# Kernel optimization log

Hardware: AMD Instinct MI355X
Metric: run time of the kernel (lower is better)

Reference implementation:

```python
import jax, jax.numpy as jnp
import numpy as np

B, T, F = 64, 512, 256
ENC = 256      # encoder output dim
P = 128        # projection_dim
H = 256        # gru_hidden_dim
K = 12         # num_future_steps
TEMP = 0.1


def setup_inputs() -> dict:
    key = jax.random.key(0)
    ks = jax.random.split(key, 12)
    s = lambda *d: 1.0 / np.sqrt(d[0])
    return {
        "x_seq": jax.random.normal(ks[0], (B, T, F), jnp.float32),
        # encoder: Dense(F -> ENC)
        "W_enc": jax.random.normal(ks[1], (F, ENC), jnp.float32) * s(F),
        "b_enc": jnp.zeros((ENC,), jnp.float32),
        # projection: Dense(ENC -> P)
        "W_proj": jax.random.normal(ks[2], (ENC, P), jnp.float32) * s(ENC),
        "b_proj": jnp.zeros((P,), jnp.float32),
        # GRUCell (flax convention: input dense has bias, hidden dense bias only on n)
        "Wi": jax.random.normal(ks[3], (P, 3 * H), jnp.float32) * s(P),
        "bi": jnp.zeros((3 * H,), jnp.float32),
        "Wh": jax.random.normal(ks[4], (H, 3 * H), jnp.float32) * s(H),
        "bhn": jnp.zeros((H,), jnp.float32),
        # K predictors: Dense(H -> P)
        "Wp": jax.random.normal(ks[5], (K, H, P), jnp.float32) * s(H),
        "bp": jnp.zeros((K, P), jnp.float32),
    }


def _gru_scan(z_seq, Wi, bi, Wh, bhn):
    # z_seq: [B, T, P] -> c_seq: [B, T, H]
    def step(h, x_t):
        gi = x_t @ Wi + bi          # [B, 3H]
        gh = h @ Wh                 # [B, 3H]
        ir, iz, inn = jnp.split(gi, 3, axis=-1)
        hr, hz, hn = jnp.split(gh, 3, axis=-1)
        r = jax.nn.sigmoid(ir + hr)
        z = jax.nn.sigmoid(iz + hz)
        n = jnp.tanh(inn + r * (hn + bhn))
        h_new = (1.0 - z) * n + z * h
        return h_new, h_new

    h0 = jnp.zeros((z_seq.shape[0], Wh.shape[0]), z_seq.dtype)
    _, c = jax.lax.scan(step, h0, jnp.swapaxes(z_seq, 0, 1))  # c: [T, B, H]
    return jnp.swapaxes(c, 0, 1)


def reference(x_seq, W_enc, b_enc, W_proj, b_proj, Wi, bi, Wh, bhn, Wp, bp):
    # encoder per timestep (vmap(vmap(Dense)) == batched matmul)
    z_seq = x_seq @ W_enc + b_enc                 # [B, T, ENC]
    z_seq = z_seq @ W_proj + b_proj               # [B, T, P]
    c_seq = _gru_scan(z_seq, Wi, bi, Wh, bhn)     # [B, T, H]

    Tlen = z_seq.shape[1]
    loss = jnp.asarray(0.0, z_seq.dtype)
    for k in range(1, K + 1):
        if Tlen - k <= 0:
            continue
        z_pos = z_seq[:, k:]                      # [B, T-k, P]
        pred = c_seq[:, :-k] @ Wp[k - 1] + bp[k - 1]  # [B, T-k, P]
        logits = jnp.einsum('btd,bkd->btk', pred, z_pos) / TEMP
        labels = jnp.arange(logits.shape[1])
        # NOTE: faithful to source: [..., labels] with labels=arange is an
        # identity gather along the last axis (not a diagonal pick).
        loss = loss + jnp.mean(-jax.nn.log_softmax(logits, axis=-1)[..., labels])
    return loss / K
```

## Files before the change

kernel.cpp:

```cpp
#include <hip/hip_runtime.h>
#include <hip/hip_bf16.h>
#include <math.h>

#define B_   64
#define T_   512
#define F_   256
#define ENC_ 256
#define P_   128
#define H_   256
#define K_   12
#define INV_TEMP 10.0f

typedef unsigned short u16;
typedef _Float16 half2v __attribute__((ext_vector_type(2)));
union U2H { unsigned int u; half2v h; };
typedef __attribute__((ext_vector_type(8))) short bf16x8;
typedef __attribute__((ext_vector_type(4))) float f32x4;
typedef _Float16 f16x8 __attribute__((ext_vector_type(8)));
union BF8 { bf16x8 v; u16 e[8]; };

__device__ __forceinline__ float rcpf(float x) {
#if __has_builtin(__builtin_amdgcn_rcpf)
    return __builtin_amdgcn_rcpf(x);
#else
    return 1.f / x;
#endif
}
__device__ __forceinline__ u16 f2bf(float f) {
    unsigned int u = __float_as_uint(f);
    unsigned int r = (u + 0x7fffu + ((u >> 16) & 1u)) >> 16;
    return (u16)r;
}
__device__ __forceinline__ float bf2f(u16 v) {
    return __uint_as_float(((unsigned int)v) << 16);
}
__device__ __forceinline__ float bflo(unsigned int u) { return __uint_as_float(u << 16); }
__device__ __forceinline__ float bfhi(unsigned int u) { return __uint_as_float(u & 0xffff0000u); }
__device__ __forceinline__ float wave_sum(float v) {
    #pragma unroll
    for (int o = 32; o > 0; o >>= 1) v += __shfl_down(v, o, 64);
    return v;
}

__global__ __launch_bounds__(256) void setup_conv(const float* __restrict__ Wh,
                                                  _Float16* __restrict__ Wht,
                                                  const float* __restrict__ Wi,
                                                  u16* __restrict__ Wit,
                                                  const float* __restrict__ Wp,
                                                  u16* __restrict__ Wpt,
                                                  const float* __restrict__ We,
                                                  const float* __restrict__ be,
                                                  const float* __restrict__ Wpj,
                                                  const float* __restrict__ bpj,
                                                  u16* __restrict__ Wct,
                                                  float* __restrict__ bc,
                                                  float* __restrict__ accum) {
    int bid = blockIdx.x;
    if (bid < 192) {
        __shared__ float tile0[32][33];
        int g0 = (bid % 24) * 32, k0 = (bid / 24) * 32;
        int tx = threadIdx.x & 31, ty = threadIdx.x >> 5;
        #pragma unroll
        for (int i = 0; i < 32; i += 8)
            tile0[ty + i][tx] = Wh[(size_t)(k0 + ty + i) * 768 + g0 + tx];
        __syncthreads();
        #pragma unroll
        for (int i = 0; i < 32; i += 8)
            Wht[(size_t)(g0 + ty + i) * 256 + k0 + tx] = (_Float16)tile0[tx][ty + i];
    } else if (bid < 288) {
        __shared__ float tile[32][33];
        int b2 = bid - 192;
        int n0 = (b2 % 24) * 32, k0 = (b2 / 24) * 32;
        int tx = threadIdx.x & 31, ty = threadIdx.x >> 5;
        #pragma unroll
        for (int i = 0; i < 32; i += 8)
            tile[ty + i][tx] = Wi[(size_t)(k0 + ty + i) * 768 + n0 + tx];
        __syncthreads();
        #pragma unroll
        for (int i = 0; i < 32; i += 8)
            Wit[(size_t)(n0 + ty + i) * 128 + k0 + tx] = f2bf(tile[tx][ty + i]);
    } else if (bid < 672) {
        __shared__ float tile2[32][33];
        int b3 = bid - 288;
        int kq = b3 / 32, rem = b3 % 32;
        int h0 = (rem % 8) * 32, p0 = (rem / 8) * 32;
        int tx = threadIdx.x & 31, ty = threadIdx.x >> 5;
        #pragma unroll
        for (int i = 0; i < 32; i += 8)
            tile2[ty + i][tx] = Wp[(size_t)kq * H_ * P_ + (size_t)(h0 + ty + i) * P_ + p0 + tx];
        __syncthreads();
        #pragma unroll
        for (int i = 0; i < 32; i += 8)
            Wpt[(size_t)kq * P_ * H_ + (size_t)(p0 + ty + i) * H_ + h0 + tx] = f2bf(tile2[tx][ty + i]);
    } else {
        int f = (bid - 672) * 2 + (threadIdx.x >> 7);
        int p = threadIdx.x & 127;
        if (f < F_) {
            float a = 0.f;
            for (int e = 0; e < ENC_; e++) a = fmaf(We[f * ENC_ + e], Wpj[e * P_ + p], a);
            Wct[(size_t)p * F_ + f] = f2bf(a);
        } else if (f == F_) {
            float a = bpj[p];
            for (int e = 0; e < ENC_; e++) a = fmaf(be[e], Wpj[e * P_ + p], a);
            bc[p] = a;
        } else {
            #pragma unroll
            for (int i = 0; i < 8; i++) accum[p * 8 + i] = 0.f;
        }
    }
}

__global__ __launch_bounds__(256) void gemm_mfma_f32a(const float* __restrict__ A,
                                                      const u16* __restrict__ Bt,
                                                      const float* __restrict__ bias,
                                                      u16* __restrict__ Ch,
                                                      int N, int K) {
    int tid  = threadIdx.x;
    int w    = tid >> 6;
    int lane = tid & 63;
    int col  = lane & 15;
    int quad = lane >> 4;
    int bm = blockIdx.y * 64, bn = blockIdx.x * 128;

    f32x4 acc[8] = {};
    const float* arow = A + (size_t)(bm + w * 16 + col) * K;
    #pragma unroll
    for (int k0 = 0; k0 < K; k0 += 32) {
        float4 v0 = *(const float4*)(arow + k0 + quad * 8);
        float4 v1 = *(const float4*)(arow + k0 + quad * 8 + 4);
        BF8 af;
        af.e[0] = f2bf(v0.x); af.e[1] = f2bf(v0.y); af.e[2] = f2bf(v0.z); af.e[3] = f2bf(v0.w);
        af.e[4] = f2bf(v1.x); af.e[5] = f2bf(v1.y); af.e[6] = f2bf(v1.z); af.e[7] = f2bf(v1.w);
        #pragma unroll
        for (int nt = 0; nt < 8; nt++) {
            bf16x8 bf = *(const bf16x8*)(Bt + (size_t)(bn + nt * 16 + col) * K + k0 + quad * 8);
            acc[nt] = __builtin_amdgcn_mfma_f32_16x16x32_bf16(af.v, bf, acc[nt], 0, 0, 0);
        }
    }
    #pragma unroll
    for (int nt = 0; nt < 8; nt++) {
        int gn = bn + nt * 16 + col;
        float bv = bias[gn];
        #pragma unroll
        for (int r = 0; r < 4; r++) {
            int gm = bm + w * 16 + quad * 4 + r;
            Ch[(size_t)gm * N + gn] = f2bf(acc[nt][r] + bv);
        }
    }
}

__global__ __launch_bounds__(256) void gemm_mfma(const u16* __restrict__ A,
                                                 const u16* __restrict__ Bt,
                                                 const float* __restrict__ bias,
                                                 u16* __restrict__ Ch,
                                                 int N, int K) {
    int tid  = threadIdx.x;
    int w    = tid >> 6;
    int lane = tid & 63;
    int col  = lane & 15;
    int quad = lane >> 4;
    int bm = blockIdx.y * 64, bn = blockIdx.x * 128;

    f32x4 acc[8] = {};
    const u16* arow = A + (size_t)(bm + w * 16 + col) * K;
    #pragma unroll
    for (int k0 = 0; k0 < K; k0 += 32) {
        bf16x8 af = *(const bf16x8*)(arow + k0 + quad * 8);
        #pragma unroll
        for (int nt = 0; nt < 8; nt++) {
            bf16x8 bf = *(const bf16x8*)(Bt + (size_t)(bn + nt * 16 + col) * K + k0 + quad * 8);
            acc[nt] = __builtin_amdgcn_mfma_f32_16x16x32_bf16(af, bf, acc[nt], 0, 0, 0);
        }
    }
    #pragma unroll
    for (int nt = 0; nt < 8; nt++) {
        int gn = bn + nt * 16 + col;
        float bv = bias[gn];
        #pragma unroll
        for (int r = 0; r < 4; r++) {
            int gm = bm + w * 16 + quad * 4 + r;
            Ch[(size_t)gm * N + gn] = f2bf(acc[nt][r] + bv);
        }
    }
}

#define GRUB_ 64

__global__ __attribute__((amdgpu_flat_work_group_size(512, 512)))
void gru_zsum_kernel(const u16* __restrict__ gi,
                     const _Float16* __restrict__ Wht,
                     const float* __restrict__ bhn,
                     u16* __restrict__ ch,
                     const u16* __restrict__ zh,
                     float* __restrict__ zsum) {
    __shared__ __align__(16) char smem[8704];
    int tid = threadIdx.x;

    if (blockIdx.x >= GRUB_) {
        float (*part)[128] = (float (*)[128])smem;
        int b   = blockIdx.x - GRUB_;
        int pg  = tid & 31;
        int g   = tid >> 5;
        const u16* zb = zh + (size_t)b * T_ * P_;
        float s0 = 0.f, s1 = 0.f, s2 = 0.f, s3 = 0.f;
        for (int t = 1 + g; t < T_; t += 16) {
            uint2 v = *(const uint2*)(zb + (size_t)t * P_ + pg * 4);
            s0 += bflo(v.x); s1 += bfhi(v.x);
            s2 += bflo(v.y); s3 += bfhi(v.y);
        }
        part[g][pg * 4 + 0] = s0; part[g][pg * 4 + 1] = s1;
        part[g][pg * 4 + 2] = s2; part[g][pg * 4 + 3] = s3;
        __syncthreads();
        if (tid < 128) {
            float s = 0.f;
            #pragma unroll
            for (int g2 = 0; g2 < 16; g2++) s += part[g2][tid];
            zsum[(size_t)b * P_ + tid] = s;
        }
        return;
    }

    _Float16* hbase = (_Float16*)smem;

    int lane = tid & 63, w = tid >> 6;
    int col  = lane & 15, quad = lane >> 4;
    int b    = blockIdx.x;
    int jj0  = w * 32 + col;

    f16x8 wf[3][2][8];
    #pragma unroll
    for (int g = 0; g < 3; g++)
        #pragma unroll
        for (int n2 = 0; n2 < 2; n2++) {
            const _Float16* src = Wht + (size_t)(g * 256 + jj0 + n2 * 16) * 256 + quad * 8;
            #pragma unroll
            for (int k0 = 0; k0 < 8; k0++)
                wf[g][n2][k0] = *(const f16x8*)(src + k0 * 32);
        }
    #pragma unroll
    for (int g = 0; g < 3; g++)
        #pragma unroll
        for (int n2 = 0; n2 < 2; n2++)
            #pragma unroll
            for (int k0 = 0; k0 < 8; k0++)
                asm volatile("" : "+v"(wf[g][n2][k0]));

    for (int i = tid; i < 528; i += 512) hbase[i] = (_Float16)0.f;

    const u16* gb = gi + (size_t)b * T_ * 768;
    u16* cb       = ch + (size_t)b * T_ * 256;
    float bh0 = bhn[jj0], bh1 = bhn[jj0 + 16];
    float hold0 = 0.f, hold1 = 0.f;
    unsigned int pf[6];

    {
        pf[0] = gb[jj0];        pf[1] = gb[jj0 + 16];
        pf[2] = gb[256 + jj0];  pf[3] = gb[256 + jj0 + 16];
        pf[4] = gb[512 + jj0];  pf[5] = gb[512 + jj0 + 16];
    }
    __syncthreads();

    auto body = [&](int t, int c) {
        int n = c ^ 1;
        const _Float16* HC = hbase + c * 264;
        _Float16*       HN = hbase + n * 264;
        f32x4 aR0 = {}, aR1 = {}, aZ0 = {}, aZ1 = {}, aN0 = {}, aN1 = {};
        #pragma unroll
        for (int k0 = 0; k0 < 8; k0++) {
            f16x8 af = *(const f16x8*)(HC + k0 * 32 + quad * 8);
            aR0 = __builtin_amdgcn_mfma_f32_16x16x32_f16(af, wf[0][0][k0], aR0, 0, 0, 0);
            aR1 = __builtin_amdgcn_mfma_f32_16x16x32_f16(af, wf[0][1][k0], aR1, 0, 0, 0);
            aZ0 = __builtin_amdgcn_mfma_f32_16x16x32_f16(af, wf[1][0][k0], aZ0, 0, 0, 0);
            aZ1 = __builtin_amdgcn_mfma_f32_16x16x32_f16(af, wf[1][1][k0], aZ1, 0, 0, 0);
            aN0 = __builtin_amdgcn_mfma_f32_16x16x32_f16(af, wf[2][0][k0], aN0, 0, 0, 0);
            aN1 = __builtin_amdgcn_mfma_f32_16x16x32_f16(af, wf[2][1][k0], aN1, 0, 0, 0);
        }
        float rg0 = rcpf(1.f + __expf(-(bf2f((u16)pf[0]) + aR0[0])));
        float rg1 = rcpf(1.f + __expf(-(bf2f((u16)pf[1]) + aR1[0])));
        float zg0 = rcpf(1.f + __expf(-(bf2f((u16)pf[2]) + aZ0[0])));
        float zg1 = rcpf(1.f + __expf(-(bf2f((u16)pf[3]) + aZ1[0])));
        float xn0 = bf2f((u16)pf[4]) + rg0 * (aN0[0] + bh0);
        float xn1 = bf2f((u16)pf[5]) + rg1 * (aN1[0] + bh1);
        float nn0 = fmaf(2.f, rcpf(1.f + __expf(-2.f * xn0)), -1.f);
        float nn1 = fmaf(2.f, rcpf(1.f + __expf(-2.f * xn1)), -1.f);
        hold0 = (1.f - zg0) * nn0 + zg0 * hold0;
        hold1 = (1.f - zg1) * nn1 + zg1 * hold1;
        if (quad == 0) {
            HN[jj0]      = (_Float16)hold0;
            HN[jj0 + 16] = (_Float16)hold1;
        } else if (quad == 1) {
            u16* cr = cb + (size_t)t * 256;
            cr[jj0]      = f2bf(hold0);
            cr[jj0 + 16] = f2bf(hold1);
        }
        if (t + 1 < T_) {
            const u16* gr = gb + (size_t)(t + 1) * 768;
            pf[0] = gr[jj0];        pf[1] = gr[jj0 + 16];
            pf[2] = gr[256 + jj0];  pf[3] = gr[256 + jj0 + 16];
            pf[4] = gr[512 + jj0];  pf[5] = gr[512 + jj0 + 16];
        }
        asm volatile("s_waitcnt lgkmcnt(0)" ::: "memory");
        __builtin_amdgcn_s_barrier();
        asm volatile("" ::: "memory");
    };

    #pragma unroll 1
    for (int t = 0; t < T_; t += 2) {
        body(t,     0);
        body(t + 1, 1);
    }
}

__global__ __attribute__((amdgpu_flat_work_group_size(512, 512)))
void loss_fused(const u16* __restrict__ ch,
                const u16* __restrict__ Wpt,
                const float* __restrict__ bp,
                const u16* __restrict__ zh,
                const float* __restrict__ zsum,
                float* __restrict__ accum) {
    __shared__ u16 Pst[3][128][136];
    __shared__ u16 Zt[64][136];
    __shared__ float sS[3][128];
    __shared__ float red[8];
    int kz    = blockIdx.z;
    int kbase = 1 + kz * 3;
    int b  = blockIdx.y;
    int t0 = blockIdx.x * 128;
    int tid  = threadIdx.x;
    int w    = tid >> 6;
    int lane = tid & 63;
    int col  = lane & 15;
    int quad = lane >> 4;
    const u16* zb = zh + (size_t)b * T_ * P_;

    int row0 = tid >> 4;
    int row1 = row0 + 32;
    int off  = (tid & 15) * 8;
    uint4 rA = *(const uint4*)(zb + (size_t)(kbase + row0) * P_ + off);
    uint4 rB = *(const uint4*)(zb + (size_t)(kbase + row1) * P_ + off);

    if (tid < 128) {
        float s = zsum[(size_t)b * P_ + tid];
        for (int t = 1; t < kbase; t++) s -= bf2f(zb[(size_t)t * P_ + tid]);
        sS[0][tid] = s;
        s -= bf2f(zb[(size_t)kbase * P_ + tid]);       sS[1][tid] = s;
        s -= bf2f(zb[(size_t)(kbase + 1) * P_ + tid]); sS[2][tid] = s;
    }

    {
        f32x4 acc[3][8] = {};
        const u16* arow = ch + ((size_t)b * T_ + t0 + w * 16 + col) * H_;
        const u16* wk   = Wpt + (size_t)(kbase - 1) * P_ * H_;
        #pragma unroll
        for (int k0 = 0; k0 < 8; k0++) {
            bf16x8 af = *(const bf16x8*)(arow + k0 * 32 + quad * 8);
            #pragma unroll
            for (int j = 0; j < 3; j++)
                #pragma unroll
                for (int nt = 0; nt < 8; nt++) {
                    bf16x8 bf = *(const bf16x8*)(wk + (size_t)j * P_ * H_
                                 + (size_t)(nt * 16 + col) * H_ + k0 * 32 + quad * 8);
                    acc[j][nt] = __builtin_amdgcn_mfma_f32_16x16x32_bf16(af, bf, acc[j][nt], 0, 0, 0);
                }
        }
        #pragma unroll
        for (int j = 0; j < 3; j++)
            #pragma unroll
            for (int nt = 0; nt < 8; nt++) {
                float bias = bp[(size_t)(kbase - 1 + j) * P_ + nt * 16 + col];
                #pragma unroll
                for (int r = 0; r < 4; r++)
                    Pst[j][w * 16 + quad * 4 + r][nt * 16 + col] = f2bf(acc[j][nt][r] + bias);
            }
    }
    __syncthreads();

    float mloc[3][4], sloc[3][4];
    #pragma unroll
    for (int j = 0; j < 3; j++)
        #pragma unroll
        for (int r = 0; r < 4; r++) { mloc[j][r] = -INFINITY; sloc[j][r] = 0.f; }

    int TkMax = T_ - kbase;
    for (int ct = 0; ct < TkMax; ct += 64) {
        __syncthreads();
        *(uint4*)&Zt[row0][off] = rA;
        *(uint4*)&Zt[row1][off] = rB;
        __syncthreads();
        if (ct + 64 < TkMax) {
            int tc = kbase + ct + 64;
            rA = *(const uint4*)(zb + (size_t)(tc + row0) * P_ + off);
            rB = *(const uint4*)(zb + (size_t)(tc + row1) * P_ + off);
        }
        f32x4 acc[3][4] = {};
        #pragma unroll
        for (int k0 = 0; k0 < 4; k0++) {
            bf16x8 pa0 = *(const bf16x8*)(&Pst[0][w * 16 + col][k0 * 32 + quad * 8]);
            bf16x8 pa1 = *(const bf16x8*)(&Pst[1][w * 16 + col][k0 * 32 + quad * 8]);
            bf16x8 pa2 = *(const bf16x8*)(&Pst[2][w * 16 + col][k0 * 32 + quad * 8]);
            #pragma unroll
            for (int nt = 0; nt < 4; nt++) {
                bf16x8 bf = *(const bf16x8*)(&Zt[nt * 16 + col][k0 * 32 + quad * 8]);
                acc[0][nt] = __builtin_amdgcn_mfma_f32_16x16x32_bf16(pa0, bf, acc[0][nt], 0, 0, 0);
                acc[1][nt] = __builtin_amdgcn_mfma_f32_16x16x32_bf16(pa1, bf, acc[1][nt], 0, 0, 0);
                acc[2][nt] = __builtin_amdgcn_mfma_f32_16x16x32_bf16(pa2, bf, acc[2][nt], 0, 0, 0);
            }
        }
        #pragma unroll
        for (int j = 0; j < 3; j++) {
            #pragma unroll
            for (int r = 0; r < 4; r++) {
                float l[4];
                float tmax = -INFINITY;
                #pragma unroll
                for (int nt = 0; nt < 4; nt++) {
                    int cc = ct + nt * 16 + col;
                    bool v = (cc >= j) && (kbase + cc < T_);
                    l[nt] = v ? acc[j][nt][r] * INV_TEMP : -INFINITY;
                    tmax = fmaxf(tmax, l[nt]);
                }
                float mnew = fmaxf(mloc[j][r], tmax);
                float e = __expf(l[0] - mnew) + __expf(l[1] - mnew)
                        + __expf(l[2] - mnew) + __expf(l[3] - mnew);
                sloc[j][r] = sloc[j][r] * __expf(mloc[j][r] - mnew) + e;
                mloc[j][r] = mnew;
            }
        }
    }
    #pragma unroll
    for (int j = 0; j < 3; j++)
        #pragma unroll
        for (int r = 0; r < 4; r++) {
            #pragma unroll
            for (int o = 1; o < 16; o <<= 1) {
                float mo = __shfl_xor(mloc[j][r], o, 64);
                float so = __shfl_xor(sloc[j][r], o, 64);
                float mn = fmaxf(mloc[j][r], mo);
                sloc[j][r] = sloc[j][r] * __expf(mloc[j][r] - mn) + so * __expf(mo - mn);
                mloc[j][r] = mn;
            }
        }
    float bs = 0.f;
    #pragma unroll
    for (int j = 0; j < 3; j++) {
        int Tkj = T_ - (kbase + j);
        float tkinv = INV_TEMP / (float)Tkj;
        float scale = 1.0f / ((float)K_ * (float)B_ * (float)Tkj);
        #pragma unroll
        for (int r = 0; r < 4; r++) {
            int row = w * 16 + quad * 4 + r;
            BF8 pv;
            pv.v = *(const bf16x8*)(&Pst[j][row][col * 8]);
            float d = 0.f;
            #pragma unroll
            for (int m = 0; m < 8; m++) d = fmaf(bf2f(pv.e[m]), sS[j][col * 8 + m], d);
            #pragma unroll
            for (int o = 1; o < 16; o <<= 1) d += __shfl_xor(d, o, 64);
            int gr = t0 + row;
            if (gr < Tkj) bs += (mloc[j][r] + __logf(sloc[j][r]) - d * tkinv) * scale;
        }
    }
    if (col != 0) bs = 0.f;
    bs = wave_sum(bs);
    if (lane == 0) red[w] = bs;
    __syncthreads();
    if (tid == 0) {
        float tot = 0.f;
        #pragma unroll
        for (int i = 0; i < 8; i++) tot += red[i];
        atomicAdd(&accum[(blockIdx.x * 809 + b * 67 + blockIdx.z * 131) & 1023], tot);
    }
}

__global__ void finalize(const float* __restrict__ accum, float* __restrict__ out) {
    int tid = threadIdx.x;
    __shared__ float red[4];
    float v = 0.f;
    for (int i = tid; i < 1024; i += 256) v += accum[i];
    float sres = wave_sum(v);
    if ((tid & 63) == 0) red[tid >> 6] = sres;
    __syncthreads();
    if (tid == 0) out[0] = red[0] + red[1] + red[2] + red[3];
}

extern "C" void kernel_launch(void* const* d_in, const int* in_sizes, int n_in,
                              void* d_out, int out_size, void* d_ws, size_t ws_size,
                              hipStream_t stream) {
    const float* x      = (const float*)d_in[0];
    const float* W_enc  = (const float*)d_in[1];
    const float* b_enc  = (const float*)d_in[2];
    const float* W_proj = (const float*)d_in[3];
    const float* b_proj = (const float*)d_in[4];
    const float* Wi     = (const float*)d_in[5];
    const float* bi     = (const float*)d_in[6];
    const float* Wh     = (const float*)d_in[7];
    const float* bhn    = (const float*)d_in[8];
    const float* Wp     = (const float*)d_in[9];
    const float* bp     = (const float*)d_in[10];
    float* out = (float*)d_out;

    float* ws    = (float*)d_ws;
    float* bc    = ws;
    float* accum = bc + 128;
    _Float16* Wht = (_Float16*)(ws + 1152);
    u16* Wct     = (u16*)(ws + 99456);
    u16* Wit     = (u16*)(ws + 115840);
    u16* Wpt     = (u16*)(ws + 164992);
    u16* zh      = (u16*)(ws + 361600);
    float* zsum  = ws + 2458752;
    u16* gi      = (u16*)(ws + 2466944);
    u16* ch      = (u16*)(ws + 15049856);

    const int MT = B_ * T_;

    setup_conv<<<801, 256, 0, stream>>>(Wh, Wht, Wi, Wit, Wp, Wpt,
                                        W_enc, b_enc, W_proj, b_proj, Wct, bc, accum);
    gemm_mfma_f32a<<<dim3(1, MT / 64), 256, 0, stream>>>(x, Wct, bc, zh, P_, F_);
    gemm_mfma<<<dim3(6, MT / 64), 256, 0, stream>>>(zh, Wit, bi, gi, 3 * H_, P_);
    gru_zsum_kernel<<<GRUB_ + B_, 512, 0, stream>>>(gi, Wht, bhn, ch, zh, zsum);
    loss_fused<<<dim3(4, B_, 4), 512, 0, stream>>>(ch, Wpt, bp, zh, zsum, accum);
    finalize<<<1, 256, 0, stream>>>(accum, out);
}
```

Before: 1.040 ms.

## Restructure loss kernel to one block per (batch, k) with register-held predictions

The loss kernel's work split changes. Before, each block handled three k values for a 128-row chunk of t. Now each block handles one (batch, k) pair and all 512 rows, keeping the projected prediction fragments for four row-chunks in registers. Each loaded z tile is then reused across all rows, so z is streamed once per (b,k) instead of once per 128-row chunk, and the z tile is double-buffered in shared memory. The cost is more registers (pfrag, 16 accumulators, softmax state), which may lower occupancy, and a smaller grid of 768 blocks.

```diff
diff --git a/kernel.cpp b/kernel.cpp
--- a/kernel.cpp
+++ b/kernel.cpp
@@ -318,14 +318,14 @@
                 const u16* __restrict__ zh,
                 const float* __restrict__ zsum,
                 float* __restrict__ accum) {
-    __shared__ u16 Pst[3][128][136];
-    __shared__ u16 Zt[64][136];
-    __shared__ float sS[3][128];
+    __shared__ u16 Pst[128][136];
+    __shared__ u16 Zt[2][64][136];
+    __shared__ float sS[128];
     __shared__ float red[8];
-    int kz    = blockIdx.z;
-    int kbase = 1 + kz * 3;
-    int b  = blockIdx.y;
-    int t0 = blockIdx.x * 128;
+    int b  = blockIdx.x;
+    int kz = blockIdx.y;
+    int k  = kz + 1;
+    int Tk = T_ - k;
     int tid  = threadIdx.x;
     int w    = tid >> 6;
     int lane = tid & 63;
@@ -333,81 +333,100 @@
     int quad = lane >> 4;
     const u16* zb = zh + (size_t)b * T_ * P_;
 
-    int row0 = tid >> 4;
-    int row1 = row0 + 32;
-    int off  = (tid & 15) * 8;
-    uint4 rA = *(const uint4*)(zb + (size_t)(kbase + row0) * P_ + off);
-    uint4 rB = *(const uint4*)(zb + (size_t)(kbase + row1) * P_ + off);
-
     if (tid < 128) {
         float s = zsum[(size_t)b * P_ + tid];
-        for (int t = 1; t < kbase; t++) s -= bf2f(zb[(size_t)t * P_ + tid]);
-        sS[0][tid] = s;
-        s -= bf2f(zb[(size_t)kbase * P_ + tid]);       sS[1][tid] = s;
-        s -= bf2f(zb[(size_t)(kbase + 1) * P_ + tid]); sS[2][tid] = s;
-    }
-
-    {
-        f32x4 acc[3][8] = {};
-        const u16* arow = ch + ((size_t)b * T_ + t0 + w * 16 + col) * H_;
-        const u16* wk   = Wpt + (size_t)(kbase - 1) * P_ * H_;
+        for (int t = 1; t < k; t++) s -= bf2f(zb[(size_t)t * P_ + tid]);
+        sS[tid] = s;
+    }
+
+    bf16x8 pfrag[4][4];
+    float  dreg[4][4];
+    const u16* wk = Wpt + (size_t)kz * P_ * H_;
+    #pragma unroll
+    for (int c = 0; c < 4; c++) {
+        f32x4 acc[8] = {};
+        const u16* arow = ch + ((size_t)b * T_ + c * 128 + w * 16 + col) * H_;
         #pragma unroll
         for (int k0 = 0; k0 < 8; k0++) {
             bf16x8 af = *(const bf16x8*)(arow + k0 * 32 + quad * 8);
             #pragma unroll
-            for (int j = 0; j < 3; j++)
-                #pragma unroll
-                for (int nt = 0; nt < 8; nt++) {
-                    bf16x8 bf = *(const bf16x8*)(wk + (size_t)j * P_ * H_
-                                 + (size_t)(nt * 16 + col) * H_ + k0 * 32 + quad * 8);
-                    acc[j][nt] = __builtin_amdgcn_mfma_f32_16x16x32_bf16(af, bf, acc[j][nt], 0, 0, 0);
-                }
-        }
-        #pragma unroll
-        for (int j = 0; j < 3; j++)
-            #pragma unroll
             for (int nt = 0; nt < 8; nt++) {
-                float bias = bp[(size_t)(kbase - 1 + j) * P_ + nt * 16 + col];
-                #pragma unroll
-                for (int r = 0; r < 4; r++)
-                    Pst[j][w * 16 + quad * 4 + r][nt * 16 + col] = f2bf(acc[j][nt][r] + bias);
+                bf16x8 bf = *(const bf16x8*)(wk + (size_t)(nt * 16 + col) * H_ + k0 * 32 + quad * 8);
+                acc[nt] = __builtin_amdgcn_mfma_f32_16x16x32_bf16(af, bf, acc[nt], 0, 0, 0);
             }
-    }
+        }
+        __syncthreads();
+        #pragma unroll
+        for (int nt = 0; nt < 8; nt++) {
+            float bias = bp[(size_t)kz * P_ + nt * 16 + col];
+            #pragma unroll
+            for (int r = 0; r < 4; r++)
+                Pst[w * 16 + quad * 4 + r][nt * 16 + col] = f2bf(acc[nt][r] + bias);
+        }
+        __syncthreads();
+        #pragma unroll
+        for (int k0 = 0; k0 < 4; k0++)
+            pfrag[c][k0] = *(const bf16x8*)(&Pst[w * 16 + col][k0 * 32 + quad * 8]);
+        #pragma unroll
+        for (int r = 0; r < 4; r++) {
+            BF8 pv;
+            pv.v = *(const bf16x8*)(&Pst[w * 16 + quad * 4 + r][col * 8]);
+            float d = 0.f;
+            #pragma unroll
+            for (int m = 0; m < 8; m++) d = fmaf(bf2f(pv.e[m]), sS[col * 8 + m], d);
+            #pragma unroll
+            for (int o = 1; o < 16; o <<= 1) d += __shfl_xor(d, o, 64);
+            dreg[c][r] = d;
+        }
+    }
+
+    float mloc[4][4], sloc[4][4];
+    #pragma unroll
+    for (int c = 0; c < 4; c++)
+        #pragma unroll
+        for (int r = 0; r < 4; r++) { mloc[c][r] = -INFINITY; sloc[c][r] = 0.f; }
+
+    int rr  = tid >> 4;
+    int off = (tid & 15) * 8;
+    const u16* zk = zb + (size_t)k * P_;
+    {
+        uint4 a0 = *(const uint4*)(zk + (size_t)rr * P_ + off);
+        uint4 b0 = *(const uint4*)(zk + (size_t)(rr + 32) * P_ + off);
+        *(uint4*)&Zt[0][rr][off]      = a0;
+        *(uint4*)&Zt[0][rr + 32][off] = b0;
+    }
+    uint4 rA = *(const uint4*)(zk + (size_t)(64 + rr) * P_ + off);
+    uint4 rB = *(const uint4*)(zk + (size_t)(64 + rr + 32) * P_ + off);
     __syncthreads();
 
-    float mloc[3][4], sloc[3][4];
-    #pragma unroll
-    for (int j = 0; j < 3; j++)
-        #pragma unroll
-        for (int r = 0; r < 4; r++) { mloc[j][r] = -INFINITY; sloc[j][r] = 0.f; }
-
-    int TkMax = T_ - kbase;
-    for (int ct = 0; ct < TkMax; ct += 64) {
-        __syncthreads();
-        *(uint4*)&Zt[row0][off] = rA;
-        *(uint4*)&Zt[row1][off] = rB;
-        __syncthreads();
-        if (ct + 64 < TkMax) {
-            int tc = kbase + ct + 64;
-            rA = *(const uint4*)(zb + (size_t)(tc + row0) * P_ + off);
-            rB = *(const uint4*)(zb + (size_t)(tc + row1) * P_ + off);
-        }
-        f32x4 acc[3][4] = {};
+    int cb = 0;
+    #pragma unroll 1
+    for (int it = 0; it < 8; ++it) {
+        const u16* ztb = &Zt[cb][0][0];
+        f32x4 acc[4][4] = {};
         #pragma unroll
         for (int k0 = 0; k0 < 4; k0++) {
-            bf16x8 pa0 = *(const bf16x8*)(&Pst[0][w * 16 + col][k0 * 32 + quad * 8]);
-            bf16x8 pa1 = *(const bf16x8*)(&Pst[1][w * 16 + col][k0 * 32 + quad * 8]);
-            bf16x8 pa2 = *(const bf16x8*)(&Pst[2][w * 16 + col][k0 * 32 + quad * 8]);
             #pragma unroll
             for (int nt = 0; nt < 4; nt++) {
-                bf16x8 bf = *(const bf16x8*)(&Zt[nt * 16 + col][k0 * 32 + quad * 8]);
-                acc[0][nt] = __builtin_amdgcn_mfma_f32_16x16x32_bf16(pa0, bf, acc[0][nt], 0, 0, 0);
-                acc[1][nt] = __builtin_amdgcn_mfma_f32_16x16x32_bf16(pa1, bf, acc[1][nt], 0, 0, 0);
-                acc[2][nt] = __builtin_amdgcn_mfma_f32_16x16x32_bf16(pa2, bf, acc[2][nt], 0, 0, 0);
+                bf16x8 bf = *(const bf16x8*)(ztb + (size_t)(nt * 16 + col) * 136 + k0 * 32 + quad * 8);
+                acc[0][nt] = __builtin_amdgcn_mfma_f32_16x16x32_bf16(pfrag[0][k0], bf, acc[0][nt], 0, 0, 0);
+                acc[1][nt] = __builtin_amdgcn_mfma_f32_16x16x32_bf16(pfrag[1][k0], bf, acc[1][nt], 0, 0, 0);
+                acc[2][nt] = __builtin_amdgcn_mfma_f32_16x16x32_bf16(pfrag[2][k0], bf, acc[2][nt], 0, 0, 0);
+                acc[3][nt] = __builtin_amdgcn_mfma_f32_16x16x32_bf16(pfrag[3][k0], bf, acc[3][nt], 0, 0, 0);
             }
         }
-        #pragma unroll
-        for (int j = 0; j < 3; j++) {
+        if (it < 7) {
+            *(uint4*)&Zt[cb ^ 1][rr][off]      = rA;
+            *(uint4*)&Zt[cb ^ 1][rr + 32][off] = rB;
+            if (it < 6) {
+                const u16* zn = zk + (size_t)((it + 2) * 64) * P_;
+                rA = *(const uint4*)(zn + (size_t)rr * P_ + off);
+                rB = *(const uint4*)(zn + (size_t)(rr + 32) * P_ + off);
+            }
+        }
+        int ct = it * 64;
+        #pragma unroll
+        for (int c = 0; c < 4; c++) {
             #pragma unroll
             for (int r = 0; r < 4; r++) {
                 float l[4];
@@ -415,51 +434,43 @@
                 #pragma unroll
                 for (int nt = 0; nt < 4; nt++) {
                     int cc = ct + nt * 16 + col;
-                    bool v = (cc >= j) && (kbase + cc < T_);
-                    l[nt] = v ? acc[j][nt][r] * INV_TEMP : -INFINITY;
+                    l[nt] = (cc < Tk) ? acc[c][nt][r] * INV_TEMP : -INFINITY;
                     tmax = fmaxf(tmax, l[nt]);
                 }
-                float mnew = fmaxf(mloc[j][r], tmax);
+                float mnew = fmaxf(mloc[c][r], tmax);
                 float e = __expf(l[0] - mnew) + __expf(l[1] - mnew)
                         + __expf(l[2] - mnew) + __expf(l[3] - mnew);
-                sloc[j][r] = sloc[j][r] * __expf(mloc[j][r] - mnew) + e;
-                mloc[j][r] = mnew;
+                sloc[c][r] = sloc[c][r] * __expf(mloc[c][r] - mnew) + e;
+                mloc[c][r] = mnew;
             }
         }
-    }
-    #pragma unroll
-    for (int j = 0; j < 3; j++)
+        __syncthreads();
+        cb ^= 1;
+    }
+
+    #pragma unroll
+    for (int c = 0; c < 4; c++)
         #pragma unroll
         for (int r = 0; r < 4; r++) {
             #pragma unroll
             for (int o = 1; o < 16; o <<= 1) {
-                float mo = __shfl_xor(mloc[j][r], o, 64);
-                float so = __shfl_xor(sloc[j][r], o, 64);
-                float mn = fmaxf(mloc[j][r], mo);
-                sloc[j][r] = sloc[j][r] * __expf(mloc[j][r] - mn) + so * __expf(mo - mn);
-                mloc[j][r] = mn;
+                float mo = __shfl_xor(mloc[c][r], o, 64);
+                float so = __shfl_xor(sloc[c][r], o, 64);
+                float mn = fmaxf(mloc[c][r], mo);
+                sloc[c][r] = sloc[c][r] * __expf(mloc[c][r] - mn) + so * __expf(mo - mn);
+                mloc[c][r] = mn;
             }
         }
+    float tkinv = INV_TEMP / (float)Tk;
+    float scale = 1.0f / ((float)K_ * (float)B_ * (float)Tk);
     float bs = 0.f;
     #pragma unroll
-    for (int j = 0; j < 3; j++) {
-        int Tkj = T_ - (kbase + j);
-        float tkinv = INV_TEMP / (float)Tkj;
-        float scale = 1.0f / ((float)K_ * (float)B_ * (float)Tkj);
+    for (int c = 0; c < 4; c++)
         #pragma unroll
         for (int r = 0; r < 4; r++) {
-            int row = w * 16 + quad * 4 + r;
-            BF8 pv;
-            pv.v = *(const bf16x8*)(&Pst[j][row][col * 8]);
-            float d = 0.f;
-            #pragma unroll
-            for (int m = 0; m < 8; m++) d = fmaf(bf2f(pv.e[m]), sS[j][col * 8 + m], d);
-            #pragma unroll
-            for (int o = 1; o < 16; o <<= 1) d += __shfl_xor(d, o, 64);
-            int gr = t0 + row;
-            if (gr < Tkj) bs += (mloc[j][r] + __logf(sloc[j][r]) - d * tkinv) * scale;
-        }
-    }
+            int gr = c * 128 + w * 16 + quad * 4 + r;
+            if (gr < Tk) bs += mloc[c][r] + __logf(sloc[c][r]) - dreg[c][r] * tkinv;
+        }
     if (col != 0) bs = 0.f;
     bs = wave_sum(bs);
     if (lane == 0) red[w] = bs;
@@ -468,7 +479,7 @@
         float tot = 0.f;
         #pragma unroll
         for (int i = 0; i < 8; i++) tot += red[i];
-        atomicAdd(&accum[(blockIdx.x * 809 + b * 67 + blockIdx.z * 131) & 1023], tot);
+        atomicAdd(&accum[(b * 67 + kz * 131) & 1023], tot * scale);
     }
 }
 
@@ -518,6 +529,6 @@
     gemm_mfma_f32a<<<dim3(1, MT / 64), 256, 0, stream>>>(x, Wct, bc, zh, P_, F_);
     gemm_mfma<<<dim3(6, MT / 64), 256, 0, stream>>>(zh, Wit, bi, gi, 3 * H_, P_);
     gru_zsum_kernel<<<GRUB_ + B_, 512, 0, stream>>>(gi, Wht, bhn, ch, zh, zsum);
-    loss_fused<<<dim3(4, B_, 4), 512, 0, stream>>>(ch, Wpt, bp, zh, zsum, accum);
+    loss_fused<<<dim3(B_, K_), 512, 0, stream>>>(ch, Wpt, bp, zh, zsum, accum);
     finalize<<<1, 256, 0, stream>>>(accum, out);
 }
```

After: 1.044 ms. No clear change (+0.3%).
